# Performance work log

Measured on AMD Instinct MI355X. Metric: run time of the kernel, lower is better.

The kernel has to match this reference:

```python
import jax, jax.numpy as jnp
import numpy as np

B, S, D_IN, D_OUT, H = 2, 2048, 1024, 1024, 16
HEAD = D_OUT // H

def setup_inputs() -> dict:
    key = jax.random.key(0)
    ks = jax.random.split(key, 5)
    scale = 0.02
    return {
        "x": jax.random.normal(ks[0], (B, S, D_IN), dtype=jnp.float32),
        "Wq": jax.random.normal(ks[1], (D_OUT, D_IN), dtype=jnp.float32) * scale,
        "Wk": jax.random.normal(ks[2], (D_OUT, D_IN), dtype=jnp.float32) * scale,
        "Wv": jax.random.normal(ks[3], (D_OUT, D_IN), dtype=jnp.float32) * scale,
        "Wo": jax.random.normal(ks[4], (D_OUT, D_OUT), dtype=jnp.float32) * scale,
        "bo": jnp.zeros((D_OUT,), dtype=jnp.float32),
    }

def reference(x, Wq, Wk, Wv, Wo, bo):
    b, n, _ = x.shape
    # linear projections (torch Linear: y = x @ W.T)
    q = (x @ Wq.T).reshape(b, n, H, HEAD).transpose(0, 2, 1, 3)  # [b,h,n,d]
    k = (x @ Wk.T).reshape(b, n, H, HEAD).transpose(0, 2, 1, 3)
    v = (x @ Wv.T).reshape(b, n, H, HEAD).transpose(0, 2, 1, 3)
    scores = jnp.einsum('bhqd,bhkd->bhqk', q, k)  # [b,h,n,n]
    causal = jnp.triu(jnp.ones((n, n), dtype=bool), k=1)
    scores = jnp.where(causal, -jnp.inf, scores)
    # NOTE: original scales by sqrt(d_out**0.5) == d_out**0.25 (faithful quirk)
    inv_scale = jnp.float32(1.0 / (D_OUT ** 0.25))
    attn = jax.nn.softmax(scores * inv_scale, axis=-1)
    ctx = jnp.einsum('bhqk,bhkd->bhqd', attn, v)  # [b,h,n,d]
    ctx = ctx.transpose(0, 2, 1, 3).reshape(b, n, D_OUT)
    return ctx @ Wo.T + bo
```

## Files before the change

kernel.cpp:

```cpp
#include <hip/hip_runtime.h>

#define NB 2
#define NH 16
#define SEQ 2048
#define DM 1024
#define HD 64
#define MT (NB * SEQ)

typedef __attribute__((ext_vector_type(8))) short bf16x8;
typedef __attribute__((ext_vector_type(4))) float f32x4;
typedef __attribute__((ext_vector_type(8))) unsigned short ushort8;

__device__ __forceinline__ unsigned short f2bf(float f) {
  union { float f; unsigned u; } v; v.f = f;
  return (unsigned short)((v.u + 0x7fffu + ((v.u >> 16) & 1u)) >> 16);
}

__device__ __forceinline__ void gld_lds16(const unsigned short* g, unsigned short* l) {
  __builtin_amdgcn_global_load_lds((const __attribute__((address_space(1))) unsigned int*)g,
                                   (__attribute__((address_space(3))) unsigned int*)l, 16, 0, 0);
}

__global__ __launch_bounds__(256) void cvt_all(const float* __restrict__ x,
                                               const float* __restrict__ wq,
                                               const float* __restrict__ wk,
                                               const float* __restrict__ wv,
                                               const float* __restrict__ wo,
                                               unsigned short* __restrict__ dst) {
  const int XO = (MT * DM) / 8;
  const int WO = (DM * DM) / 8;
  int i = blockIdx.x * 256 + threadIdx.x;
  const float* src; int base;
  if (i < XO)               { src = x;  base = 0; }
  else if (i < XO + WO)     { src = wq; base = XO; }
  else if (i < XO + 2 * WO) { src = wk; base = XO + WO; }
  else if (i < XO + 3 * WO) { src = wv; base = XO + 2 * WO; }
  else                      { src = wo; base = XO + 3 * WO; }
  const float4* s4 = (const float4*)(src) + (size_t)(i - base) * 2;
  float4 f0 = s4[0], f1 = s4[1];
  ushort8 u;
  u[0] = f2bf(f0.x); u[1] = f2bf(f0.y); u[2] = f2bf(f0.z); u[3] = f2bf(f0.w);
  u[4] = f2bf(f1.x); u[5] = f2bf(f1.y); u[6] = f2bf(f1.z); u[7] = f2bf(f1.w);
  *((ushort8*)dst + i) = u;
}

__device__ __forceinline__ void gemm_bt_mainloop(const unsigned short* __restrict__ A,
                                                 const unsigned short* __restrict__ B,
                                                 int K,
                                                 unsigned short* As, unsigned short* Bs,
                                                 f32x4 acc[4][4]) {
  int tid = threadIdx.x;
  int lane = tid & 63, l15 = lane & 15, quad = lane >> 4;
  int w = tid >> 6, wm = (w >> 1) * 64, wn = (w & 1) * 64;
  int gofs[4];
#pragma unroll
  for (int it = 0; it < 4; ++it) {
    int c = tid + it * 256;
    int r = c >> 3, pos = c & 7;
    gofs[it] = r * K + ((pos ^ (r & 7)) * 8);
  }
  for (int k0 = 0; k0 < K; k0 += 64) {
#pragma unroll
    for (int it = 0; it < 4; ++it)
      gld_lds16(A + k0 + gofs[it], As + (tid + it * 256) * 8);
#pragma unroll
    for (int it = 0; it < 4; ++it)
      gld_lds16(B + k0 + gofs[it], Bs + (tid + it * 256) * 8);
    __syncthreads();
    bf16x8 a[4][2], b[4][2];
#pragma unroll
    for (int i = 0; i < 4; ++i) {
      int row = wm + i * 16 + l15, sw = row & 7;
#pragma unroll
      for (int s = 0; s < 2; ++s)
        a[i][s] = *(const bf16x8*)(As + row * 64 + (((quad + 4 * s) ^ sw) * 8));
    }
#pragma unroll
    for (int i = 0; i < 4; ++i) {
      int row = wn + i * 16 + l15, sw = row & 7;
#pragma unroll
      for (int s = 0; s < 2; ++s)
        b[i][s] = *(const bf16x8*)(Bs + row * 64 + (((quad + 4 * s) ^ sw) * 8));
    }
#pragma unroll
    for (int s = 0; s < 2; ++s)
#pragma unroll
      for (int i = 0; i < 4; ++i)
#pragma unroll
        for (int jj = 0; jj < 4; ++jj)
          acc[i][jj] = __builtin_amdgcn_mfma_f32_16x16x32_bf16(a[i][s], b[jj][s], acc[i][jj], 0, 0, 0);
    __syncthreads();
  }
}

#define QSCALE 0.2550565444f

__global__ __launch_bounds__(256, 3) void gemm_qkv(const unsigned short* __restrict__ xb,
                                                   const unsigned short* __restrict__ wcat,
                                                   unsigned short* __restrict__ qb,
                                                   unsigned short* __restrict__ kb,
                                                   unsigned short* __restrict__ vtb) {
  __shared__ unsigned short As[128 * 64], Bs[128 * 64];
  int m0 = blockIdx.y * 128, n0 = blockIdx.x * 128;
  f32x4 acc[4][4];
#pragma unroll
  for (int i = 0; i < 4; ++i)
#pragma unroll
    for (int j = 0; j < 4; ++j) acc[i][j] = (f32x4){0.f, 0.f, 0.f, 0.f};

  gemm_bt_mainloop(xb + (size_t)m0 * DM, wcat + (size_t)n0 * DM, DM, As, Bs, acc);

  int tid = threadIdx.x, lane = tid & 63, l15 = lane & 15, quad = lane >> 4;
  int w = tid >> 6, wm = (w >> 1) * 64, wn = (w & 1) * 64;
  int mat = n0 >> 10;
#pragma unroll
  for (int i = 0; i < 4; ++i) {
    int mbase = m0 + wm + i * 16 + quad * 4;
    int bi = mbase >> 11, s = mbase & 2047;
#pragma unroll
    for (int j = 0; j < 4; ++j) {
      int n = n0 + wn + j * 16 + l15;
      int c = n & 1023, h = c >> 6, d = c & 63;
      if (mat == 2) {
        ushort4 u;
        u.x = f2bf(acc[i][j][0]); u.y = f2bf(acc[i][j][1]);
        u.z = f2bf(acc[i][j][2]); u.w = f2bf(acc[i][j][3]);
        *(ushort4*)(vtb + ((size_t)((bi * NH + h) * HD + d)) * SEQ + s) = u;
      } else {
        unsigned short* dst = (mat == 0) ? qb : kb;
        float sc = (mat == 0) ? QSCALE : 1.0f;
#pragma unroll
        for (int reg = 0; reg < 4; ++reg)
          dst[((size_t)((bi * NH + h) * SEQ + (s + reg))) * HD + d] = f2bf(acc[i][j][reg] * sc);
      }
    }
  }
}

#define LP 136
#define LDK 72
#define LV 136

__global__ __launch_bounds__(512, 4) void attn_kernel(const unsigned short* __restrict__ qb,
                                                      const unsigned short* __restrict__ kb,
                                                      const unsigned short* __restrict__ vtb,
                                                      unsigned short* __restrict__ ctx) {
  __shared__ unsigned short Ps[128 * LP];
  __shared__ unsigned short Ks[128 * LDK];
  __shared__ unsigned short Vts[64 * LV];
  int bx = blockIdx.x, h = blockIdx.y, bi = blockIdx.z;
  int qst = bi ? (15 - bx) : bx;
  int q0 = qst * 128;
  int tid = threadIdx.x, lane = tid & 63, l15 = lane & 15, quad = lane >> 4, w = tid >> 6;

  const unsigned short* qbase = qb + ((size_t)(bi * NH + h) * SEQ + q0) * HD;
  const unsigned short* kbase = kb + ((size_t)(bi * NH + h) * SEQ) * HD;
  const unsigned short* vbase = vtb + ((size_t)(bi * NH + h) * HD) * SEQ;

  {
    int c = tid, r = c >> 3, cc = (c & 7) * 8;
    *(int4*)(Ps + r * LP + cc) = *(const int4*)(qbase + (size_t)r * HD + cc);
    c = tid + 512; r = c >> 3; cc = (c & 7) * 8;
    *(int4*)(Ps + r * LP + cc) = *(const int4*)(qbase + (size_t)r * HD + cc);
  }
  int kr = tid >> 3, kc = (tid & 7) * 8;
  int vr = tid >> 4, vc = (tid & 15) * 8;
  const unsigned short* kS0 = kbase + (size_t)kr * HD + kc;
  const unsigned short* kS1 = kS0 + (size_t)64 * HD;
  const unsigned short* vS0 = vbase + (size_t)vr * SEQ + vc;
  const unsigned short* vS1 = vS0 + (size_t)32 * SEQ;
  int4 kreg0 = *(const int4*)kS0, kreg1 = *(const int4*)kS1;
  int4 vreg0 = *(const int4*)vS0, vreg1 = *(const int4*)vS1;
  unsigned short* Kd0 = Ks + kr * LDK + kc;
  unsigned short* Kd1 = Kd0 + 64 * LDK;
  unsigned short* Vd0 = Vts + vr * LV + vc;
  unsigned short* Vd1 = Vd0 + 32 * LV;
  __syncthreads();

  bf16x8 aq0 = *(const bf16x8*)(Ps + (w * 16 + l15) * LP + 8 * quad);
  bf16x8 aq1 = *(const bf16x8*)(Ps + (w * 16 + l15) * LP + 32 + 8 * quad);

  f32x4 Oacc[4];
#pragma unroll
  for (int i = 0; i < 4; ++i) Oacc[i] = (f32x4){0.f, 0.f, 0.f, 0.f};
  float l_p[4] = {0.f, 0.f, 0.f, 0.f};
  int q0w = q0 + w * 16;
  int nt = qst + 1;
  unsigned short* Prow = Ps + (w * 16 + quad * 4) * LP + l15;

  for (int j = 0; j < nt; ++j) {
    int kv0 = j * 128;
    __syncthreads();
    *(int4*)Kd0 = kreg0; *(int4*)Kd1 = kreg1;
    *(int4*)Vd0 = vreg0; *(int4*)Vd1 = vreg1;
    __syncthreads();
    if (j + 1 < nt) {
      size_t ko = (size_t)(j + 1) * 128 * HD;
      int vo = (j + 1) * 128;
      kreg0 = *(const int4*)(kS0 + ko); kreg1 = *(const int4*)(kS1 + ko);
      vreg0 = *(const int4*)(vS0 + vo); vreg1 = *(const int4*)(vS1 + vo);
    }
    bool diag = (j == nt - 1);
    int ns_hi = diag ? w : 7;
    int s_hi = ns_hi >> 1;

    if (!diag) {
#pragma unroll
      for (int ns = 0; ns < 8; ++ns) {
        bf16x8 bk0 = *(const bf16x8*)(Ks + (ns * 16 + l15) * LDK + 8 * quad);
        bf16x8 bk1 = *(const bf16x8*)(Ks + (ns * 16 + l15) * LDK + 32 + 8 * quad);
        f32x4 s = (f32x4){0.f, 0.f, 0.f, 0.f};
        s = __builtin_amdgcn_mfma_f32_16x16x32_bf16(aq0, bk0, s, 0, 0, 0);
        s = __builtin_amdgcn_mfma_f32_16x16x32_bf16(aq1, bk1, s, 0, 0, 0);
#pragma unroll
        for (int reg = 0; reg < 4; ++reg) {
          float p = __builtin_amdgcn_exp2f(s[reg]);
          l_p[reg] += p;
          union { float f; unsigned u; } pu; pu.f = p;
          Prow[reg * LP + ns * 16] = (unsigned short)(pu.u >> 16);
        }
      }
    } else {
#pragma unroll
      for (int ns = 0; ns < 8; ++ns) {
        if (ns > ns_hi) break;
        bf16x8 bk0 = *(const bf16x8*)(Ks + (ns * 16 + l15) * LDK + 8 * quad);
        bf16x8 bk1 = *(const bf16x8*)(Ks + (ns * 16 + l15) * LDK + 32 + 8 * quad);
        f32x4 s = (f32x4){0.f, 0.f, 0.f, 0.f};
        s = __builtin_amdgcn_mfma_f32_16x16x32_bf16(aq0, bk0, s, 0, 0, 0);
        s = __builtin_amdgcn_mfma_f32_16x16x32_bf16(aq1, bk1, s, 0, 0, 0);
        bool m = (ns == ns_hi);
#pragma unroll
        for (int reg = 0; reg < 4; ++reg) {
          float xv = s[reg];
          if (m) {
            int kvg = kv0 + ns * 16 + l15;
            int qg = q0w + quad * 4 + reg;
            if (kvg > qg) xv = -INFINITY;
          }
          float p = __builtin_amdgcn_exp2f(xv);
          l_p[reg] += p;
          union { float f; unsigned u; } pu; pu.f = p;
          Prow[reg * LP + ns * 16] = (unsigned short)(pu.u >> 16);
        }
      }
      if (!(ns_hi & 1)) {
#pragma unroll
        for (int reg = 0; reg < 4; ++reg)
          Prow[reg * LP + (ns_hi + 1) * 16] = 0;
      }
    }

#pragma unroll
    for (int step = 0; step < 4; ++step) {
      if (step > s_hi) break;
      bf16x8 pa = *(const bf16x8*)(Ps + (w * 16 + l15) * LP + 8 * quad + 32 * step);
#pragma unroll
      for (int nd = 0; nd < 4; ++nd) {
        bf16x8 bv = *(const bf16x8*)(Vts + (nd * 16 + l15) * LV + 8 * quad + 32 * step);
        Oacc[nd] = __builtin_amdgcn_mfma_f32_16x16x32_bf16(pa, bv, Oacc[nd], 0, 0, 0);
      }
    }
  }

  float l_i[4];
#pragma unroll
  for (int reg = 0; reg < 4; ++reg) l_i[reg] = l_p[reg];
#pragma unroll
  for (int off = 1; off < 16; off <<= 1)
#pragma unroll
    for (int reg = 0; reg < 4; ++reg)
      l_i[reg] += __shfl_xor(l_i[reg], off, 64);
  float rl[4];
#pragma unroll
  for (int reg = 0; reg < 4; ++reg) rl[reg] = 1.0f / l_i[reg];
#pragma unroll
  for (int nd = 0; nd < 4; ++nd)
#pragma unroll
    for (int reg = 0; reg < 4; ++reg) {
      int s = q0w + quad * 4 + reg;
      int col = h * HD + nd * 16 + l15;
      ctx[((size_t)(bi * SEQ + s)) * DM + col] = f2bf(Oacc[nd][reg] * rl[reg]);
    }
}

__global__ __launch_bounds__(256, 3) void gemm_out(const unsigned short* __restrict__ ctx,
                                                   const unsigned short* __restrict__ wob,
                                                   const float* __restrict__ bo,
                                                   float* __restrict__ out) {
  __shared__ unsigned short As[128 * 64], Bs[128 * 64];
  int m0 = blockIdx.y * 128, n0 = blockIdx.x * 128;
  f32x4 acc[4][4];
#pragma unroll
  for (int i = 0; i < 4; ++i)
#pragma unroll
    for (int j = 0; j < 4; ++j) acc[i][j] = (f32x4){0.f, 0.f, 0.f, 0.f};

  gemm_bt_mainloop(ctx + (size_t)m0 * DM, wob + (size_t)n0 * DM, DM, As, Bs, acc);

  int tid = threadIdx.x, lane = tid & 63, l15 = lane & 15, quad = lane >> 4;
  int w = tid >> 6, wm = (w >> 1) * 64, wn = (w & 1) * 64;
#pragma unroll
  for (int i = 0; i < 4; ++i)
#pragma unroll
    for (int j = 0; j < 4; ++j) {
      int n = n0 + wn + j * 16 + l15;
      float bias = bo[n];
#pragma unroll
      for (int reg = 0; reg < 4; ++reg) {
        int m = m0 + wm + i * 16 + quad * 4 + reg;
        out[(size_t)m * DM + n] = acc[i][j][reg] + bias;
      }
    }
}

extern "C" void kernel_launch(void* const* d_in, const int* in_sizes, int n_in,
                              void* d_out, int out_size, void* d_ws, size_t ws_size,
                              hipStream_t stream) {
  const float* x  = (const float*)d_in[0];
  const float* Wq = (const float*)d_in[1];
  const float* Wk = (const float*)d_in[2];
  const float* Wv = (const float*)d_in[3];
  const float* Wo = (const float*)d_in[4];
  const float* bo = (const float*)d_in[5];
  float* out = (float*)d_out;

  unsigned short* ws = (unsigned short*)d_ws;
  unsigned short* xb   = ws;
  unsigned short* ctx  = ws;
  unsigned short* wcat = ws + (size_t)MT * DM;
  unsigned short* wob  = wcat + (size_t)3 * DM * DM;
  unsigned short* qb   = wob + (size_t)DM * DM;
  unsigned short* kb   = qb + (size_t)MT * DM;
  unsigned short* vtb  = kb + (size_t)MT * DM;

  int total8 = (MT * DM + 4 * DM * DM) / 8;
  cvt_all<<<total8 / 256, 256, 0, stream>>>(x, Wq, Wk, Wv, Wo, ws);

  gemm_qkv<<<dim3(24, 32), 256, 0, stream>>>(xb, wcat, qb, kb, vtb);
  attn_kernel<<<dim3(16, NH, NB), 512, 0, stream>>>(qb, kb, vtb, ctx);
  gemm_out<<<dim3(8, 32), 256, 0, stream>>>(ctx, wob, bo, out);
}
```

Before: 172.1 us.

## Retile QKV and output GEMMs, swap MFMA operands, compute softmax row sums via MFMA

The QKV GEMM now runs with 2 waves per 128x128 tile, each wave owning 64x128, with swapped MFMA operands so results come out transposed and Q/K can be stored as vector ushort4. The output GEMM switches to 64x128 tiles, doubling the grid, and writes float4 results with a vectorized bias load. In attention, the per-element row-sum accumulation and the cross-lane shuffle reduction are replaced by an MFMA against a ones vector, and the context store is vectorized. The cost is more registers per wave in the QKV GEMM and V-transpose stores that are now scalar.

```diff
diff --git a/kernel.cpp b/kernel.cpp
--- a/kernel.cpp
+++ b/kernel.cpp
@@ -44,94 +44,81 @@
   *((ushort8*)dst + i) = u;
 }
 
-__device__ __forceinline__ void gemm_bt_mainloop(const unsigned short* __restrict__ A,
-                                                 const unsigned short* __restrict__ B,
-                                                 int K,
-                                                 unsigned short* As, unsigned short* Bs,
-                                                 f32x4 acc[4][4]) {
-  int tid = threadIdx.x;
-  int lane = tid & 63, l15 = lane & 15, quad = lane >> 4;
-  int w = tid >> 6, wm = (w >> 1) * 64, wn = (w & 1) * 64;
-  int gofs[4];
-#pragma unroll
-  for (int it = 0; it < 4; ++it) {
-    int c = tid + it * 256;
-    int r = c >> 3, pos = c & 7;
-    gofs[it] = r * K + ((pos ^ (r & 7)) * 8);
-  }
-  for (int k0 = 0; k0 < K; k0 += 64) {
-#pragma unroll
-    for (int it = 0; it < 4; ++it)
-      gld_lds16(A + k0 + gofs[it], As + (tid + it * 256) * 8);
-#pragma unroll
-    for (int it = 0; it < 4; ++it)
-      gld_lds16(B + k0 + gofs[it], Bs + (tid + it * 256) * 8);
-    __syncthreads();
-    bf16x8 a[4][2], b[4][2];
-#pragma unroll
-    for (int i = 0; i < 4; ++i) {
-      int row = wm + i * 16 + l15, sw = row & 7;
-#pragma unroll
-      for (int s = 0; s < 2; ++s)
-        a[i][s] = *(const bf16x8*)(As + row * 64 + (((quad + 4 * s) ^ sw) * 8));
-    }
-#pragma unroll
-    for (int i = 0; i < 4; ++i) {
-      int row = wn + i * 16 + l15, sw = row & 7;
-#pragma unroll
-      for (int s = 0; s < 2; ++s)
-        b[i][s] = *(const bf16x8*)(Bs + row * 64 + (((quad + 4 * s) ^ sw) * 8));
-    }
-#pragma unroll
-    for (int s = 0; s < 2; ++s)
-#pragma unroll
-      for (int i = 0; i < 4; ++i)
-#pragma unroll
-        for (int jj = 0; jj < 4; ++jj)
-          acc[i][jj] = __builtin_amdgcn_mfma_f32_16x16x32_bf16(a[i][s], b[jj][s], acc[i][jj], 0, 0, 0);
-    __syncthreads();
-  }
-}
-
 #define QSCALE 0.2550565444f
 
-__global__ __launch_bounds__(256, 3) void gemm_qkv(const unsigned short* __restrict__ xb,
+__global__ __launch_bounds__(128, 2) void gemm_qkv(const unsigned short* __restrict__ xb,
                                                    const unsigned short* __restrict__ wcat,
                                                    unsigned short* __restrict__ qb,
                                                    unsigned short* __restrict__ kb,
                                                    unsigned short* __restrict__ vtb) {
   __shared__ unsigned short As[128 * 64], Bs[128 * 64];
   int m0 = blockIdx.y * 128, n0 = blockIdx.x * 128;
-  f32x4 acc[4][4];
-#pragma unroll
-  for (int i = 0; i < 4; ++i)
-#pragma unroll
-    for (int j = 0; j < 4; ++j) acc[i][j] = (f32x4){0.f, 0.f, 0.f, 0.f};
-
-  gemm_bt_mainloop(xb + (size_t)m0 * DM, wcat + (size_t)n0 * DM, DM, As, Bs, acc);
-
-  int tid = threadIdx.x, lane = tid & 63, l15 = lane & 15, quad = lane >> 4;
-  int w = tid >> 6, wm = (w >> 1) * 64, wn = (w & 1) * 64;
+  int tid = threadIdx.x, lane = tid & 63, l15 = lane & 15, quad = lane >> 4, w = tid >> 6;
+  const unsigned short* A = xb + (size_t)m0 * DM;
+  const unsigned short* B = wcat + (size_t)n0 * DM;
+
+  int gofs[8];
+#pragma unroll
+  for (int it = 0; it < 8; ++it) {
+    int c = tid + it * 128;
+    int r = c >> 3, pos = c & 7;
+    gofs[it] = r * DM + ((pos ^ (r & 7)) * 8);
+  }
+
+  f32x4 acc[8][4];
+#pragma unroll
+  for (int j = 0; j < 8; ++j)
+#pragma unroll
+    for (int i = 0; i < 4; ++i) acc[j][i] = (f32x4){0.f, 0.f, 0.f, 0.f};
+
+  for (int k0 = 0; k0 < DM; k0 += 64) {
+#pragma unroll
+    for (int it = 0; it < 8; ++it)
+      gld_lds16(A + k0 + gofs[it], As + (tid + it * 128) * 8);
+#pragma unroll
+    for (int it = 0; it < 8; ++it)
+      gld_lds16(B + k0 + gofs[it], Bs + (tid + it * 128) * 8);
+    __syncthreads();
+#pragma unroll
+    for (int s = 0; s < 2; ++s) {
+      bf16x8 fa[4];
+#pragma unroll
+      for (int i = 0; i < 4; ++i) {
+        int row = w * 64 + i * 16 + l15, sw = row & 7;
+        fa[i] = *(const bf16x8*)(As + row * 64 + (((quad + 4 * s) ^ sw) * 8));
+      }
+#pragma unroll
+      for (int j = 0; j < 8; ++j) {
+        int row = j * 16 + l15, sw = row & 7;
+        bf16x8 fb = *(const bf16x8*)(Bs + row * 64 + (((quad + 4 * s) ^ sw) * 8));
+#pragma unroll
+        for (int i = 0; i < 4; ++i)
+          acc[j][i] = __builtin_amdgcn_mfma_f32_16x16x32_bf16(fb, fa[i], acc[j][i], 0, 0, 0);
+      }
+    }
+    __syncthreads();
+  }
+
   int mat = n0 >> 10;
 #pragma unroll
-  for (int i = 0; i < 4; ++i) {
-    int mbase = m0 + wm + i * 16 + quad * 4;
-    int bi = mbase >> 11, s = mbase & 2047;
-#pragma unroll
-    for (int j = 0; j < 4; ++j) {
-      int n = n0 + wn + j * 16 + l15;
-      int c = n & 1023, h = c >> 6, d = c & 63;
+  for (int j = 0; j < 8; ++j) {
+#pragma unroll
+    for (int i = 0; i < 4; ++i) {
+      int n = n0 + j * 16 + quad * 4;
+      int m = m0 + w * 64 + i * 16 + l15;
+      int bi = m >> 11, s = m & 2047;
+      int c = n & 1023, h = c >> 6, d0 = c & 63;
       if (mat == 2) {
-        ushort4 u;
-        u.x = f2bf(acc[i][j][0]); u.y = f2bf(acc[i][j][1]);
-        u.z = f2bf(acc[i][j][2]); u.w = f2bf(acc[i][j][3]);
-        *(ushort4*)(vtb + ((size_t)((bi * NH + h) * HD + d)) * SEQ + s) = u;
+#pragma unroll
+        for (int reg = 0; reg < 4; ++reg)
+          vtb[((size_t)((bi * NH + h) * HD + d0 + reg)) * SEQ + s] = f2bf(acc[j][i][reg]);
       } else {
         unsigned short* dst = (mat == 0) ? qb : kb;
         float sc = (mat == 0) ? QSCALE : 1.0f;
-#pragma unroll
-        for (int reg = 0; reg < 4; ++reg)
-          dst[((size_t)((bi * NH + h) * SEQ + (s + reg))) * HD + d] = f2bf(acc[i][j][reg] * sc);
+        ushort4 u;
+        u.x = f2bf(acc[j][i][0] * sc); u.y = f2bf(acc[j][i][1] * sc);
+        u.z = f2bf(acc[j][i][2] * sc); u.w = f2bf(acc[j][i][3] * sc);
+        *(ushort4*)(dst + ((size_t)((bi * NH + h) * SEQ + s)) * HD + d0) = u;
       }
     }
   }
@@ -180,16 +167,19 @@
   bf16x8 aq0 = *(const bf16x8*)(Ps + (w * 16 + l15) * LP + 8 * quad);
   bf16x8 aq1 = *(const bf16x8*)(Ps + (w * 16 + l15) * LP + 32 + 8 * quad);
 
+  union { uint4 q; bf16x8 v; } onesu;
+  onesu.q = make_uint4(0x3F803F80u, 0x3F803F80u, 0x3F803F80u, 0x3F803F80u);
+  const bf16x8 ones = onesu.v;
+
   f32x4 Oacc[4];
 #pragma unroll
   for (int i = 0; i < 4; ++i) Oacc[i] = (f32x4){0.f, 0.f, 0.f, 0.f};
-  float l_p[4] = {0.f, 0.f, 0.f, 0.f};
+  f32x4 lacc = (f32x4){0.f, 0.f, 0.f, 0.f};
   int q0w = q0 + w * 16;
   int nt = qst + 1;
   unsigned short* Prow = Ps + (w * 16 + quad * 4) * LP + l15;
 
   for (int j = 0; j < nt; ++j) {
-    int kv0 = j * 128;
     __syncthreads();
     *(int4*)Kd0 = kreg0; *(int4*)Kd1 = kreg1;
     *(int4*)Vd0 = vreg0; *(int4*)Vd1 = vreg1;
@@ -215,12 +205,12 @@
 #pragma unroll
         for (int reg = 0; reg < 4; ++reg) {
           float p = __builtin_amdgcn_exp2f(s[reg]);
-          l_p[reg] += p;
           union { float f; unsigned u; } pu; pu.f = p;
           Prow[reg * LP + ns * 16] = (unsigned short)(pu.u >> 16);
         }
       }
     } else {
+      int kv0 = j * 128;
 #pragma unroll
       for (int ns = 0; ns < 8; ++ns) {
         if (ns > ns_hi) break;
@@ -239,7 +229,6 @@
             if (kvg > qg) xv = -INFINITY;
           }
           float p = __builtin_amdgcn_exp2f(xv);
-          l_p[reg] += p;
           union { float f; unsigned u; } pu; pu.f = p;
           Prow[reg * LP + ns * 16] = (unsigned short)(pu.u >> 16);
         }
@@ -255,62 +244,94 @@
     for (int step = 0; step < 4; ++step) {
       if (step > s_hi) break;
       bf16x8 pa = *(const bf16x8*)(Ps + (w * 16 + l15) * LP + 8 * quad + 32 * step);
+      lacc = __builtin_amdgcn_mfma_f32_16x16x32_bf16(ones, pa, lacc, 0, 0, 0);
 #pragma unroll
       for (int nd = 0; nd < 4; ++nd) {
         bf16x8 bv = *(const bf16x8*)(Vts + (nd * 16 + l15) * LV + 8 * quad + 32 * step);
-        Oacc[nd] = __builtin_amdgcn_mfma_f32_16x16x32_bf16(pa, bv, Oacc[nd], 0, 0, 0);
-      }
-    }
-  }
-
-  float l_i[4];
-#pragma unroll
-  for (int reg = 0; reg < 4; ++reg) l_i[reg] = l_p[reg];
-#pragma unroll
-  for (int off = 1; off < 16; off <<= 1)
-#pragma unroll
-    for (int reg = 0; reg < 4; ++reg)
-      l_i[reg] += __shfl_xor(l_i[reg], off, 64);
-  float rl[4];
-#pragma unroll
-  for (int reg = 0; reg < 4; ++reg) rl[reg] = 1.0f / l_i[reg];
-#pragma unroll
-  for (int nd = 0; nd < 4; ++nd)
-#pragma unroll
-    for (int reg = 0; reg < 4; ++reg) {
-      int s = q0w + quad * 4 + reg;
-      int col = h * HD + nd * 16 + l15;
-      ctx[((size_t)(bi * SEQ + s)) * DM + col] = f2bf(Oacc[nd][reg] * rl[reg]);
-    }
-}
-
-__global__ __launch_bounds__(256, 3) void gemm_out(const unsigned short* __restrict__ ctx,
+        Oacc[nd] = __builtin_amdgcn_mfma_f32_16x16x32_bf16(bv, pa, Oacc[nd], 0, 0, 0);
+      }
+    }
+  }
+
+  float rl = 1.0f / lacc[0];
+  int s = q0w + l15;
+#pragma unroll
+  for (int nd = 0; nd < 4; ++nd) {
+    ushort4 u;
+    u.x = f2bf(Oacc[nd][0] * rl); u.y = f2bf(Oacc[nd][1] * rl);
+    u.z = f2bf(Oacc[nd][2] * rl); u.w = f2bf(Oacc[nd][3] * rl);
+    *(ushort4*)(ctx + ((size_t)(bi * SEQ + s)) * DM + h * HD + nd * 16 + quad * 4) = u;
+  }
+}
+
+__global__ __launch_bounds__(256, 2) void gemm_out(const unsigned short* __restrict__ ctx,
                                                    const unsigned short* __restrict__ wob,
                                                    const float* __restrict__ bo,
                                                    float* __restrict__ out) {
-  __shared__ unsigned short As[128 * 64], Bs[128 * 64];
-  int m0 = blockIdx.y * 128, n0 = blockIdx.x * 128;
-  f32x4 acc[4][4];
-#pragma unroll
-  for (int i = 0; i < 4; ++i)
-#pragma unroll
-    for (int j = 0; j < 4; ++j) acc[i][j] = (f32x4){0.f, 0.f, 0.f, 0.f};
-
-  gemm_bt_mainloop(ctx + (size_t)m0 * DM, wob + (size_t)n0 * DM, DM, As, Bs, acc);
-
-  int tid = threadIdx.x, lane = tid & 63, l15 = lane & 15, quad = lane >> 4;
-  int w = tid >> 6, wm = (w >> 1) * 64, wn = (w & 1) * 64;
-#pragma unroll
-  for (int i = 0; i < 4; ++i)
-#pragma unroll
-    for (int j = 0; j < 4; ++j) {
-      int n = n0 + wn + j * 16 + l15;
-      float bias = bo[n];
-#pragma unroll
-      for (int reg = 0; reg < 4; ++reg) {
-        int m = m0 + wm + i * 16 + quad * 4 + reg;
-        out[(size_t)m * DM + n] = acc[i][j][reg] + bias;
-      }
+  __shared__ unsigned short As[64 * 64], Bs[128 * 64];
+  int m0 = blockIdx.y * 64, n0 = blockIdx.x * 128;
+  int tid = threadIdx.x, lane = tid & 63, l15 = lane & 15, quad = lane >> 4, w = tid >> 6;
+  int wm = (w >> 1) * 32, wn = (w & 1) * 64;
+  const unsigned short* A = ctx + (size_t)m0 * DM;
+  const unsigned short* B = wob + (size_t)n0 * DM;
+
+  int goA[2], goB[4];
+#pragma unroll
+  for (int it = 0; it < 2; ++it) {
+    int c = tid + it * 256, r = c >> 3, pos = c & 7;
+    goA[it] = r * DM + ((pos ^ (r & 7)) * 8);
+  }
+#pragma unroll
+  for (int it = 0; it < 4; ++it) {
+    int c = tid + it * 256, r = c >> 3, pos = c & 7;
+    goB[it] = r * DM + ((pos ^ (r & 7)) * 8);
+  }
+
+  f32x4 acc[4][2];
+#pragma unroll
+  for (int j = 0; j < 4; ++j)
+#pragma unroll
+    for (int i = 0; i < 2; ++i) acc[j][i] = (f32x4){0.f, 0.f, 0.f, 0.f};
+
+  for (int k0 = 0; k0 < DM; k0 += 64) {
+#pragma unroll
+    for (int it = 0; it < 2; ++it)
+      gld_lds16(A + k0 + goA[it], As + (tid + it * 256) * 8);
+#pragma unroll
+    for (int it = 0; it < 4; ++it)
+      gld_lds16(B + k0 + goB[it], Bs + (tid + it * 256) * 8);
+    __syncthreads();
+#pragma unroll
+    for (int s = 0; s < 2; ++s) {
+      bf16x8 fa[2];
+#pragma unroll
+      for (int i = 0; i < 2; ++i) {
+        int row = wm + i * 16 + l15, sw = row & 7;
+        fa[i] = *(const bf16x8*)(As + row * 64 + (((quad + 4 * s) ^ sw) * 8));
+      }
+#pragma unroll
+      for (int j = 0; j < 4; ++j) {
+        int row = wn + j * 16 + l15, sw = row & 7;
+        bf16x8 fb = *(const bf16x8*)(Bs + row * 64 + (((quad + 4 * s) ^ sw) * 8));
+#pragma unroll
+        for (int i = 0; i < 2; ++i)
+          acc[j][i] = __builtin_amdgcn_mfma_f32_16x16x32_bf16(fb, fa[i], acc[j][i], 0, 0, 0);
+      }
+    }
+    __syncthreads();
+  }
+
+#pragma unroll
+  for (int j = 0; j < 4; ++j)
+#pragma unroll
+    for (int i = 0; i < 2; ++i) {
+      int n = n0 + wn + j * 16 + quad * 4;
+      int m = m0 + wm + i * 16 + l15;
+      float4 bv = *(const float4*)(bo + n);
+      float4 o;
+      o.x = acc[j][i][0] + bv.x; o.y = acc[j][i][1] + bv.y;
+      o.z = acc[j][i][2] + bv.z; o.w = acc[j][i][3] + bv.w;
+      *(float4*)(out + (size_t)m * DM + n) = o;
     }
 }
 
@@ -337,7 +358,7 @@
   int total8 = (MT * DM + 4 * DM * DM) / 8;
   cvt_all<<<total8 / 256, 256, 0, stream>>>(x, Wq, Wk, Wv, Wo, ws);
 
-  gemm_qkv<<<dim3(24, 32), 256, 0, stream>>>(xb, wcat, qb, kb, vtb);
+  gemm_qkv<<<dim3(24, 32), 128, 0, stream>>>(xb, wcat, qb, kb, vtb);
   attn_kernel<<<dim3(16, NH, NB), 512, 0, stream>>>(qb, kb, vtb, ctx);
-  gemm_out<<<dim3(8, 32), 256, 0, stream>>>(ctx, wob, bo, out);
-}
+  gemm_out<<<dim3(8, 64), 256, 0, stream>>>(ctx, wob, bo, out);
+}
```

Result: no change. 168.8 us (-1.9%).
